# Performance work log

Measured on AMD Instinct MI355X. Metric: run time of the kernel, lower is better.

The kernel has to match this reference:

```python
import jax, jax.numpy as jnp
import numpy as np

DIM = 1024


def setup_inputs() -> dict:
    key = jax.random.key(0)
    kx, kq, kk, kv, kp = jax.random.split(key, 5)
    scale = 1.0 / np.sqrt(DIM)  # ~PyTorch Linear init scale
    return {
        "x": jax.random.normal(kx, (4, 4096, DIM), dtype=jnp.float32),
        "Wq": jax.random.normal(kq, (DIM, DIM), dtype=jnp.float32) * scale,
        "Wk": jax.random.normal(kk, (DIM, DIM), dtype=jnp.float32) * scale,
        "Wv": jax.random.normal(kv, (DIM, DIM), dtype=jnp.float32) * scale,
        "Wp": jax.random.normal(kp, (DIM, DIM), dtype=jnp.float32) * scale,
    }


def reference(x, Wq, Wk, Wv, Wp):
    # nn.Linear: y = x @ W^T (no bias)
    q = jnp.einsum("bsd,ed->bse", x, Wq)
    k = jnp.einsum("bsd,ed->bse", x, Wk)
    v = jnp.einsum("bsd,ed->bse", x, Wv)
    dim = x.shape[-1]
    # maxP 'readout' scaling: 1/dim (instead of 1/sqrt(dim))
    scores = jnp.einsum("bqd,bkd->bqk", q, k) / dim
    attn = jax.nn.softmax(scores, axis=-1)
    out = jnp.einsum("bqk,bkd->bqd", attn, v)
    return jnp.einsum("bsd,ed->bse", out, Wp)
```

## Files before the change

### kernel.cpp

```cpp
#include <hip/hip_runtime.h>

typedef unsigned short u16;
typedef __attribute__((ext_vector_type(8))) short bf16x8;
typedef __attribute__((ext_vector_type(4))) float f32x4;
typedef __attribute__((ext_vector_type(4))) unsigned short us4;
typedef __attribute__((ext_vector_type(8))) unsigned short us8;

__device__ __forceinline__ u16 f2us(float f) {
  union { float f; unsigned u; } a; a.f = f;
  unsigned u = a.u;
  u += 0x7fffu + ((u >> 16) & 1u);
  return (u16)(u >> 16);
}
__device__ __forceinline__ float us2f(u16 h) {
  union { unsigned u; float f; } a; a.u = ((unsigned)h) << 16;
  return a.f;
}

#define GLDS(g, l) __builtin_amdgcn_global_load_lds( \
    (const __attribute__((address_space(1))) void*)(g), \
    (__attribute__((address_space(3))) void*)(l), 16, 0, 0)

__global__ __launch_bounds__(256) void convert_all(
    const float* __restrict__ x, const float* __restrict__ Wq,
    const float* __restrict__ Wk, const float* __restrict__ Wv,
    const float* __restrict__ Wp, u16* __restrict__ xb, u16* __restrict__ wb) {
  const int bid = blockIdx.x;
  const float* src;
  u16* dst;
  int off;
  if (bid < 16384) {
    src = x; dst = xb; off = bid * 256 + threadIdx.x;
  } else {
    const int w = (bid - 16384) >> 10;
    const int lb = (bid - 16384) & 1023;
    src = (w == 0) ? Wq : (w == 1) ? Wk : (w == 2) ? Wv : Wp;
    dst = wb + (size_t)w * 1048576;
    off = lb * 256 + threadIdx.x;
  }
  f32x4 v = ((const f32x4*)src)[off];
  us4 o;
  o.x = f2us(v.x); o.y = f2us(v.y); o.z = f2us(v.z); o.w = f2us(v.w);
  ((us4*)dst)[off] = o;
}

#define MFMA_QUAD(QR, QC)                                                        \
  do {                                                                           \
    __builtin_amdgcn_s_setprio(1);                                               \
    _Pragma("unroll") for (int m = 0; m < 4; ++m)                                \
    _Pragma("unroll") for (int n = 0; n < 2; ++n)                                \
    _Pragma("unroll") for (int s = 0; s < 2; ++s)                                \
      acc[(QR)*4 + m][(QC)*2 + n] = __builtin_amdgcn_mfma_f32_16x16x32_bf16(     \
          af[(QR)*4 + m][s], bf[(QC)*2 + n][s], acc[(QR)*4 + m][(QC)*2 + n],     \
          0, 0, 0);                                                              \
    __builtin_amdgcn_s_setprio(0);                                               \
  } while (0)

#define STAGE_A(buf, h, kb)                                                  \
  do {                                                                       \
    const int su_ = (h) * 128 * lda + (kb);                                  \
    GLDS(Ap + aoff0 + su_, As + (buf) * 16384 + (h) * 8192 + ldst0);         \
    GLDS(Ap + aoff1 + su_, As + (buf) * 16384 + (h) * 8192 + ldst1);         \
  } while (0)

#define STAGE_B(buf, h, kb)                                                  \
  do {                                                                       \
    const int su_ = (h) * 128 * ldb + (kb);                                  \
    GLDS(Bp + boff0 + su_, Bs + (buf) * 16384 + (h) * 8192 + ldst0);         \
    GLDS(Bp + boff1 + su_, Bs + (buf) * 16384 + (h) * 8192 + ldst1);         \
  } while (0)

template <int EP>
__global__ __launch_bounds__(512, 2) void gemm256(
    const u16* __restrict__ A0, const u16* __restrict__ A1,
    const u16* __restrict__ A2, const u16* __restrict__ A3,
    const u16* __restrict__ B0, const u16* __restrict__ B1,
    const u16* __restrict__ B2, const u16* __restrict__ B3,
    void* C0, void* C1, void* C2, void* C3,
    int K, int lda, int ldb, int ldc, float scale) {
  __shared__ u16 As[32768];
  __shared__ u16 Bs[32768];
  const int tid = threadIdx.x;
  const int lane = tid & 63;
  const int wid = tid >> 6;
  const int wm = wid >> 2;
  const int wn = wid & 3;
  const int z = blockIdx.z;
  const u16* A = (z == 0) ? A0 : (z == 1) ? A1 : (z == 2) ? A2 : A3;
  const u16* B = (z == 0) ? B0 : (z == 1) ? B1 : (z == 2) ? B2 : B3;
  void* C = (z == 0) ? C0 : (z == 1) ? C1 : (z == 2) ? C2 : C3;

  const int gx = gridDim.x;
  const int nwg = gx * (int)gridDim.y;
  const int orig = (int)blockIdx.y * gx + (int)blockIdx.x;
  const int swz = (orig & 7) * (nwg >> 3) + (orig >> 3);
  const long trow = (long)(swz / gx) * 256;
  const long tcol = (long)(swz % gx) * 256;

  const int srow = tid >> 3;
  const int sgrp = (tid & 7) ^ (srow & 7);
  const int aoff0 = srow * lda + sgrp * 8;
  const int aoff1 = aoff0 + (lda << 6);
  const int boff0 = srow * ldb + sgrp * 8;
  const int boff1 = boff0 + (ldb << 6);
  const int ldst0 = (tid & ~63) * 8;
  const int ldst1 = ldst0 + 4096;
  const u16* Ap = A + trow * lda;
  const u16* Bp = B + tcol * ldb;

  const int l15x64 = (lane & 15) * 64;
  const int cs0 = ((((lane >> 4) * 8)) ^ ((lane & 7) * 8)) + l15x64;
  const int cs1 = ((32 + ((lane >> 4) * 8)) ^ ((lane & 7) * 8)) + l15x64;

  f32x4 acc[8][4];
  f32x4 zero = {0.f, 0.f, 0.f, 0.f};
#pragma unroll
  for (int m = 0; m < 8; ++m)
#pragma unroll
    for (int n = 0; n < 4; ++n) acc[m][n] = zero;

  const int NT = K >> 6;
  const int kmask = K - 1;

  STAGE_A(0, 0, 0);
  STAGE_A(0, 1, 0);
  STAGE_B(0, 0, 0);
  STAGE_B(0, 1, 0);
  STAGE_A(1, 0, 64 & kmask);
  STAGE_A(1, 1, 64 & kmask);
  asm volatile("s_waitcnt vmcnt(4)" ::: "memory");
  __builtin_amdgcn_s_barrier();

  for (int t = 0; t < NT; ++t) {
    const int cur = t & 1, nxt = cur ^ 1;
    const int kb1 = ((t + 1) << 6) & kmask;
    const int kb2 = ((t + 2) << 6) & kmask;
    const u16* Acur = As + cur * 16384 + wm * 8192;
    const u16* Bcur = Bs + cur * 16384 + (wn >> 1) * 8192 + (wn & 1) * 4096;
    bf16x8 af[8][2], bf[4][2];

#pragma unroll
    for (int m = 0; m < 4; ++m) {
      af[m][0] = *(const bf16x8*)(Acur + m * 1024 + cs0);
      af[m][1] = *(const bf16x8*)(Acur + m * 1024 + cs1);
    }
#pragma unroll
    for (int n = 0; n < 2; ++n) {
      bf[n][0] = *(const bf16x8*)(Bcur + n * 1024 + cs0);
      bf[n][1] = *(const bf16x8*)(Bcur + n * 1024 + cs1);
    }
    STAGE_B(nxt, 0, kb1);
    __builtin_amdgcn_s_barrier();
    MFMA_QUAD(0, 0);
    __builtin_amdgcn_s_barrier();

#pragma unroll
    for (int m = 0; m < 4; ++m) {
      af[4 + m][0] = *(const bf16x8*)(Acur + (4 + m) * 1024 + cs0);
      af[4 + m][1] = *(const bf16x8*)(Acur + (4 + m) * 1024 + cs1);
    }
    STAGE_B(nxt, 1, kb1);
    __builtin_amdgcn_s_barrier();
    MFMA_QUAD(1, 0);
    __builtin_amdgcn_s_barrier();

#pragma unroll
    for (int n = 0; n < 2; ++n) {
      bf[2 + n][0] = *(const bf16x8*)(Bcur + (2 + n) * 1024 + cs0);
      bf[2 + n][1] = *(const bf16x8*)(Bcur + (2 + n) * 1024 + cs1);
    }
    STAGE_A(cur, 0, kb2);
    __builtin_amdgcn_s_barrier();
    MFMA_QUAD(0, 1);
    __builtin_amdgcn_s_barrier();

    STAGE_A(cur, 1, kb2);
    __builtin_amdgcn_s_barrier();
    MFMA_QUAD(1, 1);
    asm volatile("s_waitcnt vmcnt(4)" ::: "memory");
    __builtin_amdgcn_s_barrier();
  }

  asm volatile("s_waitcnt vmcnt(0)" ::: "memory");

  if (EP == 0 || (EP == 3 && z != 2)) {
    u16* Cb = (u16*)C;
#pragma unroll
    for (int m = 0; m < 8; ++m) {
      int gr = (int)trow + wm * 128 + m * 16 + ((lane >> 4) << 2);
#pragma unroll
      for (int n = 0; n < 4; ++n) {
        int gc = (int)tcol + wn * 64 + n * 16 + (lane & 15);
        f32x4 v = acc[m][n];
#pragma unroll
        for (int j = 0; j < 4; ++j) Cb[(size_t)(gr + j) * ldc + gc] = f2us(v[j] * scale);
      }
    }
  } else if (EP == 3) {
    u16* Ct = (u16*)C;
#pragma unroll
    for (int m = 0; m < 8; ++m) {
      int gr = (int)trow + wm * 128 + m * 16 + ((lane >> 4) << 2);
      int b = gr >> 12;
      int sl = gr & 4095;
      u16* base = Ct + ((size_t)b << 22) + sl;
#pragma unroll
      for (int n = 0; n < 4; ++n) {
        int gc = (int)tcol + wn * 64 + n * 16 + (lane & 15);
        f32x4 v = acc[m][n];
        us4 o;
        o.x = f2us(v[0] * scale); o.y = f2us(v[1] * scale);
        o.z = f2us(v[2] * scale); o.w = f2us(v[3] * scale);
        *(us4*)(base + (size_t)gc * 4096) = o;
      }
    }
  } else {
    float* Cf = (float*)C;
#pragma unroll
    for (int m = 0; m < 8; ++m) {
      int gr = (int)trow + wm * 128 + m * 16 + ((lane >> 4) << 2);
#pragma unroll
      for (int n = 0; n < 4; ++n) {
        int gc = (int)tcol + wn * 64 + n * 16 + (lane & 15);
        f32x4 v = acc[m][n];
#pragma unroll
        for (int j = 0; j < 4; ++j) Cf[(size_t)(gr + j) * ldc + gc] = v[j] * scale;
      }
    }
  }
}

__global__ __launch_bounds__(256) void softmax_all(u16* S0, u16* S1, u16* S2, u16* S3) {
  const int row = blockIdx.x;
  const int b = row >> 12;
  u16* S = (b == 0) ? S0 : (b == 1) ? S1 : (b == 2) ? S2 : S3;
  const int t = threadIdx.x;
  const int lane = t & 63;
  const int wave = t >> 6;
  u16* p = S + (size_t)(row & 4095) * 4096 + t * 16;
  us8 r0 = *(const us8*)p;
  us8 r1 = *(const us8*)(p + 8);
  float f[16];
#pragma unroll
  for (int j = 0; j < 8; ++j) { f[j] = us2f(r0[j]); f[8 + j] = us2f(r1[j]); }

  float mx = f[0];
#pragma unroll
  for (int j = 1; j < 16; ++j) mx = fmaxf(mx, f[j]);
#pragma unroll
  for (int o = 32; o > 0; o >>= 1) mx = fmaxf(mx, __shfl_xor(mx, o));
  __shared__ float rmax[4], rsum[4];
  if (lane == 0) rmax[wave] = mx;
  __syncthreads();
  mx = fmaxf(fmaxf(rmax[0], rmax[1]), fmaxf(rmax[2], rmax[3]));

  float e[16], s = 0.f;
#pragma unroll
  for (int j = 0; j < 16; ++j) { e[j] = __expf(f[j] - mx); s += e[j]; }
#pragma unroll
  for (int o = 32; o > 0; o >>= 1) s += __shfl_xor(s, o);
  if (lane == 0) rsum[wave] = s;
  __syncthreads();
  s = rsum[0] + rsum[1] + rsum[2] + rsum[3];
  float inv = 1.f / s;

  us8 o0, o1;
#pragma unroll
  for (int j = 0; j < 8; ++j) { o0[j] = f2us(e[j] * inv); o1[j] = f2us(e[8 + j] * inv); }
  *(us8*)p = o0;
  *(us8*)(p + 8) = o1;
}

extern "C" void kernel_launch(void* const* d_in, const int* in_sizes, int n_in,
                              void* d_out, int out_size, void* d_ws, size_t ws_size,
                              hipStream_t stream) {
  (void)in_sizes; (void)n_in; (void)out_size;
  const float* x  = (const float*)d_in[0];
  const float* Wq = (const float*)d_in[1];
  const float* Wk = (const float*)d_in[2];
  const float* Wv = (const float*)d_in[3];
  const float* Wp = (const float*)d_in[4];

  if (ws_size < 209715200) return;
  char* ws = (char*)d_ws;
  u16* xb  = (u16*)(ws);
  u16* wqb = (u16*)(ws + 33554432);
  u16* wkb = wqb + 1048576;
  u16* wvb = wkb + 1048576;
  u16* wpb = wvb + 1048576;
  u16* Qb  = (u16*)(ws + 41943040);
  u16* Kb  = (u16*)(ws + 75497472);
  u16* Vt  = (u16*)(ws + 109051904);
  u16* Ssp = (u16*)(ws + 142606336);
  u16* O   = (u16*)(ws + 176160768);

  u16* S0 = (u16*)d_out;
  u16* S1 = S0 + 16777216;
  u16* S2 = xb;
  u16* S3 = Ssp;

  convert_all<<<20480, 256, 0, stream>>>(x, Wq, Wk, Wv, Wp, xb, wqb);

  gemm256<3><<<dim3(4, 64, 3), 512, 0, stream>>>(
      xb, xb, xb, xb, wqb, wkb, wvb, wvb, Qb, Kb, Vt, Vt,
      1024, 1024, 1024, 1024, 1.f);

  const u16 *Q0 = Qb, *Q1 = Qb + 4194304, *Q2 = Qb + 8388608, *Q3 = Qb + 12582912;
  const u16 *K0 = Kb, *K1 = Kb + 4194304, *K2 = Kb + 8388608, *K3 = Kb + 12582912;
  gemm256<0><<<dim3(16, 16, 4), 512, 0, stream>>>(Q0, Q1, Q2, Q3, K0, K1, K2, K3,
                                                  S0, S1, S2, S3, 1024, 1024, 1024, 4096,
                                                  1.f / 1024.f);

  softmax_all<<<16384, 256, 0, stream>>>(S0, S1, S2, S3);

  const u16 *V0 = Vt, *V1 = Vt + 4194304, *V2 = Vt + 8388608, *V3 = Vt + 12582912;
  u16 *O0 = O, *O1 = O + 4194304, *O2 = O + 8388608, *O3 = O + 12582912;
  gemm256<0><<<dim3(4, 16, 4), 512, 0, stream>>>(S0, S1, S2, S3, V0, V1, V2, V3,
                                                 O0, O1, O2, O3, 4096, 4096, 4096, 1024, 1.f);

  gemm256<2><<<dim3(4, 64, 1), 512, 0, stream>>>(O, O, O, O, wpb, wpb, wpb, wpb,
                                                 d_out, d_out, d_out, d_out,
                                                 1024, 1024, 1024, 1024, 1.f);
}
```

Measured before the change: 487.3 us.

## Software-pipeline LDS fragment loads across iterations in GEMM main loop

Restructures the GEMM main loop so that the A/B register fragments for the next k-tile are loaded from LDS during the last MFMA quadrant of the current tile. The quadrant order and the global-to-LDS staging order are reshuffled to match, and the vmcnt waits are adjusted. The aim is to hide LDS read latency behind matrix-core work and cut stalls at the start of each iteration. The cost is extra live fragment registers and a more fragile ordering of barriers and waits that could expose races.

```diff
diff --git a/kernel.cpp b/kernel.cpp
--- a/kernel.cpp
+++ b/kernel.cpp
@@ -44,15 +44,14 @@
   ((us4*)dst)[off] = o;
 }
 
-#define MFMA_QUAD(QR, QC)                                                        \
+#define MFMA_Q(FA, FB, QR, QC)                                                   \
   do {                                                                           \
     __builtin_amdgcn_s_setprio(1);                                               \
     _Pragma("unroll") for (int m = 0; m < 4; ++m)                                \
     _Pragma("unroll") for (int n = 0; n < 2; ++n)                                \
     _Pragma("unroll") for (int s = 0; s < 2; ++s)                                \
       acc[(QR)*4 + m][(QC)*2 + n] = __builtin_amdgcn_mfma_f32_16x16x32_bf16(     \
-          af[(QR)*4 + m][s], bf[(QC)*2 + n][s], acc[(QR)*4 + m][(QC)*2 + n],     \
-          0, 0, 0);                                                              \
+          FA[m][s], FB[n][s], acc[(QR)*4 + m][(QC)*2 + n], 0, 0, 0);             \
     __builtin_amdgcn_s_setprio(0);                                               \
   } while (0)
 
@@ -122,14 +121,29 @@
   const int NT = K >> 6;
   const int kmask = K - 1;
 
+  bf16x8 fa0[4][2], fa1[4][2], fb0[2][2], fb1[2][2];
+
   STAGE_A(0, 0, 0);
   STAGE_A(0, 1, 0);
   STAGE_B(0, 0, 0);
   STAGE_B(0, 1, 0);
   STAGE_A(1, 0, 64 & kmask);
-  STAGE_A(1, 1, 64 & kmask);
-  asm volatile("s_waitcnt vmcnt(4)" ::: "memory");
+  asm volatile("s_waitcnt vmcnt(2)" ::: "memory");
   __builtin_amdgcn_s_barrier();
+  {
+    const u16* Ac = As + wm * 8192;
+    const u16* Bc = Bs + (wn >> 1) * 8192 + (wn & 1) * 4096;
+#pragma unroll
+    for (int m = 0; m < 4; ++m) {
+      fa0[m][0] = *(const bf16x8*)(Ac + m * 1024 + cs0);
+      fa0[m][1] = *(const bf16x8*)(Ac + m * 1024 + cs1);
+    }
+#pragma unroll
+    for (int n = 0; n < 2; ++n) {
+      fb0[n][0] = *(const bf16x8*)(Bc + n * 1024 + cs0);
+      fb0[n][1] = *(const bf16x8*)(Bc + n * 1024 + cs1);
+    }
+  }
 
   for (int t = 0; t < NT; ++t) {
     const int cur = t & 1, nxt = cur ^ 1;
@@ -137,47 +151,47 @@
     const int kb2 = ((t + 2) << 6) & kmask;
     const u16* Acur = As + cur * 16384 + wm * 8192;
     const u16* Bcur = Bs + cur * 16384 + (wn >> 1) * 8192 + (wn & 1) * 4096;
-    bf16x8 af[8][2], bf[4][2];
-
+    const u16* Anxt = As + nxt * 16384 + wm * 8192;
+    const u16* Bnxt = Bs + nxt * 16384 + (wn >> 1) * 8192 + (wn & 1) * 4096;
+
+    STAGE_A(nxt, 1, kb1);
+    STAGE_B(nxt, 0, kb1);
+#pragma unroll
+    for (int n = 0; n < 2; ++n) {
+      fb1[n][0] = *(const bf16x8*)(Bcur + (2 + n) * 1024 + cs0);
+      fb1[n][1] = *(const bf16x8*)(Bcur + (2 + n) * 1024 + cs1);
+    }
+    __builtin_amdgcn_s_barrier();
+    MFMA_Q(fa0, fb0, 0, 0);
+    __builtin_amdgcn_s_barrier();
+
+    STAGE_B(nxt, 1, kb1);
 #pragma unroll
     for (int m = 0; m < 4; ++m) {
-      af[m][0] = *(const bf16x8*)(Acur + m * 1024 + cs0);
-      af[m][1] = *(const bf16x8*)(Acur + m * 1024 + cs1);
+      fa1[m][0] = *(const bf16x8*)(Acur + (4 + m) * 1024 + cs0);
+      fa1[m][1] = *(const bf16x8*)(Acur + (4 + m) * 1024 + cs1);
+    }
+    __builtin_amdgcn_s_barrier();
+    MFMA_Q(fa0, fb1, 0, 1);
+    __builtin_amdgcn_s_barrier();
+
+    MFMA_Q(fa1, fb1, 1, 1);
+    __builtin_amdgcn_s_barrier();
+
+    STAGE_A(cur, 0, kb2);
+    __builtin_amdgcn_s_barrier();
+    asm volatile("s_waitcnt vmcnt(2)" ::: "memory");
+    MFMA_Q(fa1, fb0, 1, 0);
+#pragma unroll
+    for (int m = 0; m < 4; ++m) {
+      fa0[m][0] = *(const bf16x8*)(Anxt + m * 1024 + cs0);
+      fa0[m][1] = *(const bf16x8*)(Anxt + m * 1024 + cs1);
     }
 #pragma unroll
     for (int n = 0; n < 2; ++n) {
-      bf[n][0] = *(const bf16x8*)(Bcur + n * 1024 + cs0);
-      bf[n][1] = *(const bf16x8*)(Bcur + n * 1024 + cs1);
-    }
-    STAGE_B(nxt, 0, kb1);
-    __builtin_amdgcn_s_barrier();
-    MFMA_QUAD(0, 0);
-    __builtin_amdgcn_s_barrier();
-
-#pragma unroll
-    for (int m = 0; m < 4; ++m) {
-      af[4 + m][0] = *(const bf16x8*)(Acur + (4 + m) * 1024 + cs0);
-      af[4 + m][1] = *(const bf16x8*)(Acur + (4 + m) * 1024 + cs1);
-    }
-    STAGE_B(nxt, 1, kb1);
-    __builtin_amdgcn_s_barrier();
-    MFMA_QUAD(1, 0);
-    __builtin_amdgcn_s_barrier();
-
-#pragma unroll
-    for (int n = 0; n < 2; ++n) {
-      bf[2 + n][0] = *(const bf16x8*)(Bcur + (2 + n) * 1024 + cs0);
-      bf[2 + n][1] = *(const bf16x8*)(Bcur + (2 + n) * 1024 + cs1);
-    }
-    STAGE_A(cur, 0, kb2);
-    __builtin_amdgcn_s_barrier();
-    MFMA_QUAD(0, 1);
-    __builtin_amdgcn_s_barrier();
-
-    STAGE_A(cur, 1, kb2);
-    __builtin_amdgcn_s_barrier();
-    MFMA_QUAD(1, 1);
-    asm volatile("s_waitcnt vmcnt(4)" ::: "memory");
+      fb0[n][0] = *(const bf16x8*)(Bnxt + n * 1024 + cs0);
+      fb0[n][1] = *(const bf16x8*)(Bnxt + n * 1024 + cs1);
+    }
     __builtin_amdgcn_s_barrier();
   }
 
```

Result: slower. 525.9 us (+7.9%).
